# Kernel optimization log

Measured on AMD Instinct MI355X. Metric: run time of the kernel, lower is better.

The kernel has to match this reference:

```python
import jax, jax.numpy as jnp
import numpy as np
from jax import lax

WIN = 7  # hard-coded winsize in PSF.forward
EPS = 1e-8


def _box_sum(x, n):
    # Sliding n x n window sum with zero padding (== ZeroPad2d(n//2) + unfold sum),
    return lax.reduce_window(x, 0.0, lax.add, (1, 1, n, n), (1, 1, 1, 1), 'SAME')


def _patch_stats(x, n):
    n2 = n * n
    s = _box_sum(x, n)
    s2 = _box_sum(x * x, n)
    mean = s / n2
    # torch .var() default is unbiased (divide by N-1)
    var = (s2 - n2 * mean * mean) / (n2 - 1)
    return mean, jnp.maximum(var, 0.0)


def patch_mv_norm(x, n):
    mean, var = _patch_stats(x, n)
    return (x - mean) / (jnp.sqrt(var) + EPS)


def patch_adain(x, y, n):
    x_norm = patch_mv_norm(x, n)
    y_mean, y_var = _patch_stats(y, n)
    return x_norm * jnp.sqrt(y_var) + y_mean  # note: no eps on y_std, as in source


def conv1x1(x, w, b):
    # x: (B,C,H,W), w: (O,C), b: (O,)
    return jnp.einsum('oc,bchw->bohw', w, x) + b[None, :, None, None]


def setup_inputs() -> dict:
    key = jax.random.key(0)
    ks = jax.random.split(key, 12)
    B, C, H, W = 8, 256, 128, 128
    front = jax.random.normal(ks[0], (B, C, H, W), dtype=jnp.float32)
    back = jax.random.normal(ks[1], (B, C, H, W), dtype=jnp.float32)
    mask = jax.random.uniform(ks[2], (B, 1, H, W), dtype=jnp.float32)
    scale = 0.02
    we = jax.random.normal(ks[3], (C, C), dtype=jnp.float32) * scale
    wf = jax.random.normal(ks[4], (C, C), dtype=jnp.float32) * scale
    wg = jax.random.normal(ks[5], (C, C), dtype=jnp.float32) * scale
    wh = jax.random.normal(ks[6], (C, C), dtype=jnp.float32) * scale
    be = jax.random.normal(ks[7], (C,), dtype=jnp.float32) * scale
    bf = jax.random.normal(ks[8], (C,), dtype=jnp.float32) * scale
    bg = jax.random.normal(ks[9], (C,), dtype=jnp.float32) * scale
    bh = jax.random.normal(ks[10], (C,), dtype=jnp.float32) * scale
    return {'front': front, 'back': back, 'mask': mask,
            'we': we, 'be': be, 'wf': wf, 'bf': bf,
            'wg': wg, 'bg': bg, 'wh': wh, 'bh': bh}


def reference(front, back, mask, we, be, wf, bf, wg, bg, wh, bh):
    b, c, h, w = front.shape
    EE = conv1x1(patch_adain(front, back, WIN), we, be)
    FF = conv1x1(patch_mv_norm(front, WIN), wf, bf)
    GG = conv1x1(patch_mv_norm(back, WIN), wg, bg)
    HH = conv1x1(back, wh, bh)
    # channel-wise cosine similarity between FF and GG
    F_n = jnp.sqrt(jnp.sum(FF * FF, axis=1))  # (B,H,W)
    G_n = jnp.sqrt(jnp.sum(GG * GG, axis=1))
    S = jnp.sum(FF * GG, axis=1) / (F_n * G_n)
    # per-sample spatial min-max normalization
    S_flat = S.reshape(b, h * w)
    s_min = jnp.min(S_flat, axis=1, keepdims=True)
    s_max = jnp.max(S_flat, axis=1, keepdims=True)
    S_n = ((S_flat - s_min) / (s_max - s_min)).reshape(b, 1, h, w)
    fused = S_n * EE + (1.0 - S_n) * HH
    return fused
```

## Files before the change

### kernel.cpp

```cpp
#include <hip/hip_runtime.h>
#include <math.h>

#define PIX 16384
#define TSZ ((size_t)33554432)

typedef __attribute__((ext_vector_type(8))) short  short8;
typedef __attribute__((ext_vector_type(4))) float  float4v;
typedef __attribute__((ext_vector_type(4))) unsigned int uint4v;
typedef __attribute__((ext_vector_type(2))) unsigned int uint2v;

__device__ __forceinline__ unsigned short f2bf(float x) {
  unsigned int u = __float_as_uint(x);
  u += 0x7fffu + ((u >> 16) & 1u);
  return (unsigned short)(u >> 16);
}
__device__ __forceinline__ float bf2f(unsigned short h) {
  return __uint_as_float(((unsigned int)h) << 16);
}
__device__ __forceinline__ unsigned int pack_bf2(float lo, float hi) {
  unsigned int ul = __float_as_uint(lo); ul += 0x7fffu + ((ul >> 16) & 1u);
  unsigned int uh = __float_as_uint(hi); uh += 0x7fffu + ((uh >> 16) & 1u);
  return __builtin_amdgcn_perm(uh, ul, 0x07060302u);
}

__global__ __launch_bounds__(256) void k_prep(const float* __restrict__ we,
                                              const float* __restrict__ wf,
                                              const float* __restrict__ wg,
                                              const float* __restrict__ wh,
                                              unsigned short* __restrict__ wbf) {
  int idx = blockIdx.x * 256 + threadIdx.x;
  int g = idx >> 16, within = idx & 65535;
  const float* src = (g == 0) ? wf : (g == 1) ? wg : (g == 2) ? we : wh;
  int e    = within & 7;
  int lane = (within >> 3) & 63;
  int im   = (within >> 9) & 3;
  int wv   = (within >> 11) & 3;
  int i    = within >> 13;
  int col = lane & 15, q = lane >> 4;
  int m = wv * 64 + im * 16 + col;
  int k = i * 32 + q * 8 + e;
  wbf[idx] = f2bf(src[m * 256 + k]);
}

__global__ __launch_bounds__(256, 4) void k_stats(const float* __restrict__ front,
                                                  const float* __restrict__ back,
                                                  unsigned short* __restrict__ xcm) {
  int blk = blockIdx.x;
  int s   = blk & 7;
  int c   = (blk >> 3) & 255;
  int b   = blk >> 11;
  int t   = threadIdx.x;
  int r0  = s * 16;

  __shared__ float  xs[22 * 129];
  __shared__ float2 vsp[16 * 131];
  __shared__ unsigned long long obI[16 * 64];

  size_t planeOff = ((size_t)(b * 256 + c)) * PIX;

  float meanR[8], sdR[8];

  #pragma unroll 1
  for (int phase = 0; phase < 2; ++phase) {
    const float* src = (phase == 0 ? back : front) + planeOff;
    #pragma unroll
    for (int i = 0; i < 3; ++i) {
      int idx = t + i * 256;
      if (idx < 704) {
        int l = idx >> 5, cv = (idx & 31) * 4;
        int g = r0 - 3 + l;
        float4v v = {0.f, 0.f, 0.f, 0.f};
        if (g >= 0 && g < 128) v = *(const float4v*)(src + g * 128 + cv);
        xs[l * 129 + cv]     = v[0];
        xs[l * 129 + cv + 1] = v[1];
        xs[l * 129 + cv + 2] = v[2];
        xs[l * 129 + cv + 3] = v[3];
      }
    }
    __syncthreads();
    {
      int col = t & 127;
      int rg  = (t >> 7) * 8;
      float sm = 0.f, s2 = 0.f;
      #pragma unroll
      for (int j = 0; j < 7; ++j) { float v = xs[(rg + j) * 129 + col]; sm += v; s2 = fmaf(v, v, s2); }
      vsp[rg * 131 + col] = make_float2(sm, s2);
      #pragma unroll
      for (int o = 1; o < 8; ++o) {
        float vn = xs[(rg + o + 6) * 129 + col];
        float vo = xs[(rg + o - 1) * 129 + col];
        sm += vn - vo;
        s2 += vn * vn - vo * vo;
        vsp[(rg + o) * 131 + col] = make_float2(sm, s2);
      }
    }
    __syncthreads();
    {
      int r  = t & 15;
      int c0 = (t >> 4) * 8;
      float2 w[14];
      #pragma unroll
      for (int i = 0; i < 14; ++i) {
        int cc = c0 - 3 + i;
        float2 v = make_float2(0.f, 0.f);
        if (cc >= 0 && cc < 128) v = vsp[r * 131 + cc];
        w[i] = v;
      }
      float sm = 0.f, s2 = 0.f;
      #pragma unroll
      for (int i = 0; i < 7; ++i) { sm += w[i].x; s2 += w[i].y; }
      float nrmv[8], xv[8];
      #pragma unroll
      for (int o = 0; o < 8; ++o) {
        float mean = sm * (1.f / 49.f);
        float var  = (s2 - sm * mean) * (1.f / 48.f);
        var = var > 0.f ? var : 0.f;
        float sd = __builtin_amdgcn_sqrtf(var);
        float x  = xs[(r + 3) * 129 + c0 + o];
        float nrm = (x - mean) * __builtin_amdgcn_rcpf(sd + 1e-8f);
        if (phase == 0) { meanR[o] = mean; sdR[o] = sd; }
        nrmv[o] = nrm; xv[o] = x;
        if (o < 7) { sm += w[o + 7].x - w[o].x; s2 += w[o + 7].y - w[o].y; }
      }
      #pragma unroll
      for (int op = 0; op < 4; ++op) {
        unsigned int lo32 = pack_bf2(nrmv[2 * op], nrmv[2 * op + 1]);
        float h0, h1;
        if (phase == 0) { h0 = xv[2 * op]; h1 = xv[2 * op + 1]; }
        else {
          h0 = nrmv[2 * op]     * sdR[2 * op]     + meanR[2 * op];
          h1 = nrmv[2 * op + 1] * sdR[2 * op + 1] + meanR[2 * op + 1];
        }
        unsigned int hi32 = pack_bf2(h0, h1);
        int m = (c0 >> 1) + op;
        obI[r * 64 + ((m + r) & 63)] = ((unsigned long long)hi32 << 32) | lo32;
      }
    }
    __syncthreads();
    {
      int r  = t >> 4;
      int mg = (t & 15) * 4;
      unsigned int t0[4], t1[4];
      #pragma unroll
      for (int k2 = 0; k2 < 4; ++k2) {
        unsigned long long v = obI[r * 64 + ((mg + k2 + r) & 63)];
        t0[k2] = (unsigned int)v;
        t1[k2] = (unsigned int)(v >> 32);
      }
      int p = (r0 + r) * 128 + mg * 2;
      size_t gb2 = (((size_t)(b * 256 + (p >> 6))) * 256 + c) * 64 + (p & 63);
      int tn0 = (phase == 0) ? 1 : 0;
      int tn1 = (phase == 0) ? 3 : 2;
      *(uint4v*)(xcm + (size_t)tn0 * TSZ + gb2) = (uint4v){t0[0], t0[1], t0[2], t0[3]};
      *(uint4v*)(xcm + (size_t)tn1 * TSZ + gb2) = (uint4v){t1[0], t1[1], t1[2], t1[3]};
    }
  }
}

#define SB0   __builtin_amdgcn_sched_barrier(0)
#define BARR  __builtin_amdgcn_s_barrier()
#define LGKM0 asm volatile("s_waitcnt lgkmcnt(0)" ::: "memory")
#define VMC(n) asm volatile("s_waitcnt vmcnt(" #n ")" ::: "memory")

__device__ __forceinline__ void stage_tile(const unsigned short* __restrict__ Xt,
                                           int k0, int t,
                                           unsigned short* dst) {
  int kk = ((t >> 5) << 2) + ((t & 7) >> 1);
  int px = (((t >> 3) & 3) << 4) + ((t & 1) << 3);
  const unsigned short* src = Xt + (size_t)(k0 << 6) + (kk << 6) + px;
  typedef const __attribute__((address_space(1))) unsigned int GUI;
  typedef __attribute__((address_space(3))) unsigned int LUI;
  __builtin_amdgcn_global_load_lds((GUI*)(unsigned long long)src,
                                   (LUI*)(unsigned)(unsigned long long)(dst + t * 8),
                                   16, 0, 0);
}

#define LOADA(S, I) {                                           \
  af[S][0] = *(const short8*)(Wr + (I) * 8192 + 0 * 512);       \
  af[S][1] = *(const short8*)(Wr + (I) * 8192 + 1 * 512);       \
  af[S][2] = *(const short8*)(Wr + (I) * 8192 + 2 * 512);       \
  af[S][3] = *(const short8*)(Wr + (I) * 8192 + 3 * 512); }

#define TR8(O0,O1,O2,O3,O4,O5,O6,O7)                                              \
  asm volatile("ds_read_b64_tr_b16 %0, %1 offset:" #O0 : "=v"(r0) : "v"(tra));    \
  asm volatile("ds_read_b64_tr_b16 %0, %1 offset:" #O1 : "=v"(r1) : "v"(tra));    \
  asm volatile("ds_read_b64_tr_b16 %0, %1 offset:" #O2 : "=v"(r2) : "v"(tra));    \
  asm volatile("ds_read_b64_tr_b16 %0, %1 offset:" #O3 : "=v"(r3) : "v"(tra));    \
  asm volatile("ds_read_b64_tr_b16 %0, %1 offset:" #O4 : "=v"(r4) : "v"(tra));    \
  asm volatile("ds_read_b64_tr_b16 %0, %1 offset:" #O5 : "=v"(r5) : "v"(tra));    \
  asm volatile("ds_read_b64_tr_b16 %0, %1 offset:" #O6 : "=v"(r6) : "v"(tra));    \
  asm volatile("ds_read_b64_tr_b16 %0, %1 offset:" #O7 : "=v"(r7) : "v"(tra));

#define DOMFMA(MS) {                                                        \
  union BU { unsigned u[4]; short8 s; } bu0, bu1, bu2, bu3;                 \
  bu0.u[0]=r0[0]; bu0.u[1]=r0[1]; bu0.u[2]=r1[0]; bu0.u[3]=r1[1];           \
  bu1.u[0]=r2[0]; bu1.u[1]=r2[1]; bu1.u[2]=r3[0]; bu1.u[3]=r3[1];           \
  bu2.u[0]=r4[0]; bu2.u[1]=r4[1]; bu2.u[2]=r5[0]; bu2.u[3]=r5[1];           \
  bu3.u[0]=r6[0]; bu3.u[1]=r6[1]; bu3.u[2]=r7[0]; bu3.u[3]=r7[1];           \
  short8 bv0 = bu0.s, bv1 = bu1.s, bv2 = bu2.s, bv3 = bu3.s;                \
  _Pragma("unroll")                                                         \
  for (int im = 0; im < 4; ++im) {                                          \
    acc[0][im] = __builtin_amdgcn_mfma_f32_16x16x32_bf16(af[MS][im], bv0, acc[0][im], 0, 0, 0); \
    acc[1][im] = __builtin_amdgcn_mfma_f32_16x16x32_bf16(af[MS][im], bv1, acc[1][im], 0, 0, 0); \
    acc[2][im] = __builtin_amdgcn_mfma_f32_16x16x32_bf16(af[MS][im], bv2, acc[2][im], 0, 0, 0); \
    acc[3][im] = __builtin_amdgcn_mfma_f32_16x16x32_bf16(af[MS][im], bv3, acc[3][im], 0, 0, 0); \
  } }

#define GSTEP(VN, DOSTAGE, K0, SLOT, DOA, AS, AI, MS, O0,O1,O2,O3,O4,O5,O6,O7) \
  SB0;                                                                          \
  if (DOSTAGE) stage_tile(X, K0, t, xt + (SLOT) * 2048);                        \
  SB0;                                                                          \
  if (DOA) LOADA(AS, AI);                                                       \
  SB0;                                                                          \
  VMC(VN);                                                                      \
  SB0; BARR; SB0;                                                               \
  TR8(O0,O1,O2,O3,O4,O5,O6,O7);                                                 \
  LGKM0; SB0;                                                                   \
  DOMFMA(MS);

__device__ __forceinline__ void gemm_pipe(const unsigned short* __restrict__ X,
                                          const unsigned short* __restrict__ Wm,
                                          unsigned short* xt, unsigned xbase,
                                          int mbase, int lane, int t,
                                          float4v acc[4][4]) {
  unsigned tra = xbase + (unsigned)((((lane >> 4)) << 10) + ((lane & 15) << 3));
  const unsigned short* __restrict__ Wr = Wm + ((mbase >> 6) << 11) + lane * 8;

  short8 af[3][4];
  uint2v r0, r1, r2, r3, r4, r5, r6, r7;

  #pragma unroll
  for (int in = 0; in < 4; ++in)
    #pragma unroll
    for (int im = 0; im < 4; ++im)
      acc[in][im] = (float4v){0.f, 0.f, 0.f, 0.f};

  SB0; BARR; SB0;
  stage_tile(X,  0, t, xt + 0 * 2048);
  stage_tile(X, 32, t, xt + 1 * 2048);
  stage_tile(X, 64, t, xt + 2 * 2048);
  SB0;
  LOADA(0, 0);
  SB0;
  LOADA(1, 1);
  SB0;

  GSTEP( 9,  1,  96,  3,   1, 2, 2, 0,      0,  512,  128,  640,  256,  768,  384,  896)
  GSTEP(10,  1, 128,  4,   1, 0, 3, 1,   4096, 4608, 4224, 4736, 4352, 4864, 4480, 4992)
  GSTEP(10,  1, 160,  0,   1, 1, 4, 2,   8192, 8704, 8320, 8832, 8448, 8960, 8576, 9088)
  GSTEP(10,  1, 192,  1,   1, 2, 5, 0,  12288,12800,12416,12928,12544,13056,12672,13184)
  GSTEP(10,  1, 224,  2,   1, 0, 6, 1,  16384,16896,16512,17024,16640,17152,16768,17280)
  GSTEP( 9,  0,   0,  0,   1, 1, 7, 2,      0,  512,  128,  640,  256,  768,  384,  896)
  GSTEP( 4,  0,   0,  0,   0, 0, 0, 0,   4096, 4608, 4224, 4736, 4352, 4864, 4480, 4992)
  GSTEP( 0,  0,   0,  0,   0, 0, 0, 1,   8192, 8704, 8320, 8832, 8448, 8960, 8576, 9088)
}

__global__ __launch_bounds__(256, 2) void k_gemm1(const unsigned short* __restrict__ xcm,
                                                  const unsigned short* __restrict__ wbf,
                                                  const float* __restrict__ bFF,
                                                  const float* __restrict__ bGG,
                                                  float* __restrict__ Sout) {
  int blk  = blockIdx.x;
  int b    = blk >> 8;
  int pt   = blk & 255;
  int p0   = pt * 64;
  int t    = threadIdx.x;
  int wv   = t >> 6;
  int lane = t & 63;
  int q    = lane >> 4;
  int mbase = wv * 64;

  __shared__ __align__(16) unsigned short xt[5][2048];
  __shared__ float sred[3 * 64];
  if (t < 192) sred[t] = 0.f;
  __syncthreads();
  unsigned xbase = (unsigned)(unsigned long long)&xt[0][0];

  const unsigned short* Xt = xcm + (((size_t)(b * 256 + pt)) << 14);

  float4v aF[4][4], aG[4][4];

  gemm_pipe(Xt + 0 * TSZ, wbf + 0 * 65536, &xt[0][0], xbase, mbase, lane, t, aF);
  gemm_pipe(Xt + 1 * TSZ, wbf + 1 * 65536, &xt[0][0], xbase, mbase, lane, t, aG);
  #pragma unroll
  for (int im = 0; im < 4; ++im) {
    float4v bvF = *(const float4v*)(bFF + mbase + im * 16 + q * 4);
    float4v bvG = *(const float4v*)(bGG + mbase + im * 16 + q * 4);
    #pragma unroll
    for (int in = 0; in < 4; ++in) { aF[in][im] += bvF; aG[in][im] += bvG; }
  }
  #pragma unroll
  for (int in = 0; in < 4; ++in) {
    float d = 0.f, nf = 0.f, ng = 0.f;
    #pragma unroll
    for (int im = 0; im < 4; ++im)
      #pragma unroll
      for (int r = 0; r < 4; ++r) {
        float f = aF[in][im][r], g = aG[in][im][r];
        d += f * g; nf += f * f; ng += g * g;
      }
    d  += __shfl_xor(d, 16);  d  += __shfl_xor(d, 32);
    nf += __shfl_xor(nf, 16); nf += __shfl_xor(nf, 32);
    ng += __shfl_xor(ng, 16); ng += __shfl_xor(ng, 32);
    if (lane < 16) {
      atomicAdd(&sred[0 * 64 + in * 16 + lane], d);
      atomicAdd(&sred[1 * 64 + in * 16 + lane], nf);
      atomicAdd(&sred[2 * 64 + in * 16 + lane], ng);
    }
  }
  __syncthreads();
  if (t < 64) {
    float d = sred[t], nf = sred[64 + t], ng = sred[128 + t];
    Sout[(size_t)b * PIX + p0 + t] = d / (sqrtf(nf) * sqrtf(ng));
  }
}

__global__ __launch_bounds__(256, 2) void k_gemm2(const unsigned short* __restrict__ xcm,
                                                  const unsigned short* __restrict__ wbf,
                                                  const float* __restrict__ bEE,
                                                  const float* __restrict__ bHH,
                                                  const float* __restrict__ S,
                                                  const float* __restrict__ mm,
                                                  float* __restrict__ out) {
  int blk  = blockIdx.x;
  int b    = blk >> 8;
  int pt   = blk & 255;
  int p0   = pt * 64;
  int t    = threadIdx.x;
  int wv   = t >> 6;
  int lane = t & 63;
  int col  = lane & 15;
  int q    = lane >> 4;
  int mbase = wv * 64;

  __shared__ __align__(16) unsigned short xt[5][2048];
  unsigned xbase = (unsigned)(unsigned long long)&xt[0][0];

  const unsigned short* Xt = xcm + (((size_t)(b * 256 + pt)) << 14);

  float4v aE[4][4], aH[4][4];

  gemm_pipe(Xt + 2 * TSZ, wbf + 2 * 65536, &xt[0][0], xbase, mbase, lane, t, aE);
  gemm_pipe(Xt + 3 * TSZ, wbf + 3 * 65536, &xt[0][0], xbase, mbase, lane, t, aH);

  float mn = mm[b * 2], mx = mm[b * 2 + 1];
  float inv = 1.f / (mx - mn);
  float sn[4];
  #pragma unroll
  for (int in = 0; in < 4; ++in)
    sn[in] = (S[(size_t)b * PIX + p0 + in * 16 + col] - mn) * inv;

  #pragma unroll
  for (int im = 0; im < 4; ++im) {
    float4v bvE = *(const float4v*)(bEE + mbase + im * 16 + q * 4);
    float4v bvH = *(const float4v*)(bHH + mbase + im * 16 + q * 4);
    #pragma unroll
    for (int in = 0; in < 4; ++in)
      #pragma unroll
      for (int r = 0; r < 4; ++r) {
        int m = mbase + im * 16 + q * 4 + r;
        float e = aE[in][im][r] + bvE[r];
        float h = aH[in][im][r] + bvH[r];
        out[((size_t)(b * 256 + m)) * PIX + p0 + in * 16 + col] = h + sn[in] * (e - h);
      }
  }
}

__global__ __launch_bounds__(256) void k_minmax(const float* __restrict__ S,
                                                float* __restrict__ mm) {
  int b = blockIdx.x, t = threadIdx.x;
  const float* sp = S + (size_t)b * PIX;
  float mn = 3.0e38f, mx = -3.0e38f;
  for (int i = t; i < PIX; i += 256) { float v = sp[i]; mn = fminf(mn, v); mx = fmaxf(mx, v); }
  #pragma unroll
  for (int o = 32; o >= 1; o >>= 1) {
    mn = fminf(mn, __shfl_xor(mn, o));
    mx = fmaxf(mx, __shfl_xor(mx, o));
  }
  __shared__ float smn[4], smx[4];
  if ((t & 63) == 0) { smn[t >> 6] = mn; smx[t >> 6] = mx; }
  __syncthreads();
  if (t == 0) {
    mn = fminf(fminf(smn[0], smn[1]), fminf(smn[2], smn[3]));
    mx = fmaxf(fmaxf(smx[0], smx[1]), fmaxf(smx[2], smx[3]));
    mm[b * 2] = mn; mm[b * 2 + 1] = mx;
  }
}

extern "C" void kernel_launch(void* const* d_in, const int* in_sizes, int n_in,
                              void* d_out, int out_size, void* d_ws, size_t ws_size,
                              hipStream_t stream) {
  const float* front = (const float*)d_in[0];
  const float* back  = (const float*)d_in[1];
  const float* we = (const float*)d_in[3];
  const float* be = (const float*)d_in[4];
  const float* wf = (const float*)d_in[5];
  const float* bf = (const float*)d_in[6];
  const float* wg = (const float*)d_in[7];
  const float* bg = (const float*)d_in[8];
  const float* wh = (const float*)d_in[9];
  const float* bh = (const float*)d_in[10];

  char* ws = (char*)d_ws;
  unsigned short* xcm  = (unsigned short*)(ws);
  unsigned short* wbf  = (unsigned short*)(ws + 268435456);
  float*          S    = (float*)(ws + 268959744);
  float*          mm   = (float*)(ws + 269484032);
  float*          out  = (float*)d_out;

  k_prep  <<<1024,  256, 0, stream>>>(we, wf, wg, wh, wbf);
  k_stats <<<16384, 256, 0, stream>>>(front, back, xcm);
  k_gemm1 <<<2048,  256, 0, stream>>>(xcm, wbf, bf, bg, S);
  k_minmax<<<8,     256, 0, stream>>>(S, mm);
  k_gemm2 <<<2048,  256, 0, stream>>>(xcm, wbf, be, bh, S, mm, out);
}
```

Before: 522.7 us.

## Write stats outputs directly from registers and pad box-sum buffer to drop bounds checks

In the stats kernel, the LDS staging buffer used to transpose packed bf16 outputs is removed. Each thread now packs its 8 contiguous pixels straight into 16-byte global stores. The column-sum buffer gets zero-padded halo columns, so the horizontal window loads need no bounds checks. Raw s_barrier with lgkmcnt waits replaces __syncthreads, and the occupancy hint rises from 4 to 5 blocks. The cost is a different global store pattern that may coalesce less well across a wave.

```diff
diff --git a/kernel.cpp b/kernel.cpp
--- a/kernel.cpp
+++ b/kernel.cpp
@@ -22,6 +22,11 @@
   unsigned int uh = __float_as_uint(hi); uh += 0x7fffu + ((uh >> 16) & 1u);
   return __builtin_amdgcn_perm(uh, ul, 0x07060302u);
 }
+
+#define SB0   __builtin_amdgcn_sched_barrier(0)
+#define BARR  __builtin_amdgcn_s_barrier()
+#define LGKM0 asm volatile("s_waitcnt lgkmcnt(0)" ::: "memory")
+#define VMC(n) asm volatile("s_waitcnt vmcnt(" #n ")" ::: "memory")
 
 __global__ __launch_bounds__(256) void k_prep(const float* __restrict__ we,
                                               const float* __restrict__ wf,
@@ -42,7 +47,7 @@
   wbf[idx] = f2bf(src[m * 256 + k]);
 }
 
-__global__ __launch_bounds__(256, 4) void k_stats(const float* __restrict__ front,
+__global__ __launch_bounds__(256, 5) void k_stats(const float* __restrict__ front,
                                                   const float* __restrict__ back,
                                                   unsigned short* __restrict__ xcm) {
   int blk = blockIdx.x;
@@ -53,8 +58,7 @@
   int r0  = s * 16;
 
   __shared__ float  xs[22 * 129];
-  __shared__ float2 vsp[16 * 131];
-  __shared__ unsigned long long obI[16 * 64];
+  __shared__ float2 vspD[16 * 137];
 
   size_t planeOff = ((size_t)(b * 256 + c)) * PIX;
 
@@ -77,39 +81,40 @@
         xs[l * 129 + cv + 3] = v[3];
       }
     }
-    __syncthreads();
+    LGKM0; BARR;
     {
       int col = t & 127;
       int rg  = (t >> 7) * 8;
       float sm = 0.f, s2 = 0.f;
       #pragma unroll
       for (int j = 0; j < 7; ++j) { float v = xs[(rg + j) * 129 + col]; sm += v; s2 = fmaf(v, v, s2); }
-      vsp[rg * 131 + col] = make_float2(sm, s2);
+      vspD[rg * 137 + col + 3] = make_float2(sm, s2);
       #pragma unroll
       for (int o = 1; o < 8; ++o) {
         float vn = xs[(rg + o + 6) * 129 + col];
         float vo = xs[(rg + o - 1) * 129 + col];
         sm += vn - vo;
         s2 += vn * vn - vo * vo;
-        vsp[(rg + o) * 131 + col] = make_float2(sm, s2);
+        vspD[(rg + o) * 137 + col + 3] = make_float2(sm, s2);
+      }
+      if (t < 96) {
+        int rr = t & 15;
+        int pc = t >> 4;
+        int ac = (pc < 3) ? pc : 128 + pc;
+        vspD[rr * 137 + ac] = make_float2(0.f, 0.f);
       }
     }
-    __syncthreads();
+    LGKM0; BARR;
     {
       int r  = t & 15;
       int c0 = (t >> 4) * 8;
       float2 w[14];
       #pragma unroll
-      for (int i = 0; i < 14; ++i) {
-        int cc = c0 - 3 + i;
-        float2 v = make_float2(0.f, 0.f);
-        if (cc >= 0 && cc < 128) v = vsp[r * 131 + cc];
-        w[i] = v;
-      }
+      for (int i = 0; i < 14; ++i) w[i] = vspD[r * 137 + c0 + i];
       float sm = 0.f, s2 = 0.f;
       #pragma unroll
       for (int i = 0; i < 7; ++i) { sm += w[i].x; s2 += w[i].y; }
-      float nrmv[8], xv[8];
+      float nrmv[8], hv[8];
       #pragma unroll
       for (int o = 0; o < 8; ++o) {
         float mean = sm * (1.f / 49.f);
@@ -118,49 +123,25 @@
         float sd = __builtin_amdgcn_sqrtf(var);
         float x  = xs[(r + 3) * 129 + c0 + o];
         float nrm = (x - mean) * __builtin_amdgcn_rcpf(sd + 1e-8f);
-        if (phase == 0) { meanR[o] = mean; sdR[o] = sd; }
-        nrmv[o] = nrm; xv[o] = x;
+        if (phase == 0) { meanR[o] = mean; sdR[o] = sd; hv[o] = x; }
+        else            { hv[o] = nrm * sdR[o] + meanR[o]; }
+        nrmv[o] = nrm;
         if (o < 7) { sm += w[o + 7].x - w[o].x; s2 += w[o + 7].y - w[o].y; }
       }
-      #pragma unroll
-      for (int op = 0; op < 4; ++op) {
-        unsigned int lo32 = pack_bf2(nrmv[2 * op], nrmv[2 * op + 1]);
-        float h0, h1;
-        if (phase == 0) { h0 = xv[2 * op]; h1 = xv[2 * op + 1]; }
-        else {
-          h0 = nrmv[2 * op]     * sdR[2 * op]     + meanR[2 * op];
-          h1 = nrmv[2 * op + 1] * sdR[2 * op + 1] + meanR[2 * op + 1];
-        }
-        unsigned int hi32 = pack_bf2(h0, h1);
-        int m = (c0 >> 1) + op;
-        obI[r * 64 + ((m + r) & 63)] = ((unsigned long long)hi32 << 32) | lo32;
-      }
-    }
-    __syncthreads();
-    {
-      int r  = t >> 4;
-      int mg = (t & 15) * 4;
-      unsigned int t0[4], t1[4];
-      #pragma unroll
-      for (int k2 = 0; k2 < 4; ++k2) {
-        unsigned long long v = obI[r * 64 + ((mg + k2 + r) & 63)];
-        t0[k2] = (unsigned int)v;
-        t1[k2] = (unsigned int)(v >> 32);
-      }
-      int p = (r0 + r) * 128 + mg * 2;
+      uint4v nv  = (uint4v){pack_bf2(nrmv[0], nrmv[1]), pack_bf2(nrmv[2], nrmv[3]),
+                            pack_bf2(nrmv[4], nrmv[5]), pack_bf2(nrmv[6], nrmv[7])};
+      uint4v hvv = (uint4v){pack_bf2(hv[0], hv[1]), pack_bf2(hv[2], hv[3]),
+                            pack_bf2(hv[4], hv[5]), pack_bf2(hv[6], hv[7])};
+      int p = (r0 + r) * 128 + c0;
       size_t gb2 = (((size_t)(b * 256 + (p >> 6))) * 256 + c) * 64 + (p & 63);
       int tn0 = (phase == 0) ? 1 : 0;
       int tn1 = (phase == 0) ? 3 : 2;
-      *(uint4v*)(xcm + (size_t)tn0 * TSZ + gb2) = (uint4v){t0[0], t0[1], t0[2], t0[3]};
-      *(uint4v*)(xcm + (size_t)tn1 * TSZ + gb2) = (uint4v){t1[0], t1[1], t1[2], t1[3]};
+      *(uint4v*)(xcm + (size_t)tn0 * TSZ + gb2) = nv;
+      *(uint4v*)(xcm + (size_t)tn1 * TSZ + gb2) = hvv;
     }
-  }
-}
-
-#define SB0   __builtin_amdgcn_sched_barrier(0)
-#define BARR  __builtin_amdgcn_s_barrier()
-#define LGKM0 asm volatile("s_waitcnt lgkmcnt(0)" ::: "memory")
-#define VMC(n) asm volatile("s_waitcnt vmcnt(" #n ")" ::: "memory")
+    LGKM0; BARR;
+  }
+}
 
 __device__ __forceinline__ void stage_tile(const unsigned short* __restrict__ Xt,
                                            int k0, int t,
```

New measurement: 517.4 us. No clear change (-1.0%).
